# Kernel tuning notes

Hardware: AMD Instinct MI355X
Metric: run time of the kernel (lower is better)

The kernel has to match this reference:

```python
import jax, jax.numpy as jnp
import numpy as np
from jax import lax

B = 8192      # image batch
S = 32        # seq_length
I = 16        # ltc_input_size (sensory neurons)
U = 19        # ltc_hidden_size (units)
M = 2         # num_classes (motor neurons)
UNFOLDS = 6   # ncps LTCCell default ode_unfolds
EPS = 1e-8


def setup_inputs() -> dict:
    key = jax.random.key(0)
    ks = jax.random.split(key, 24)
    u = lambda k, sh, lo, hi: jax.random.uniform(k, sh, jnp.float32, lo, hi)
    x = jax.random.normal(ks[0], (B, 1, 28, 44), jnp.float32)
    conv1_w = jax.random.normal(ks[1], (6, 1, 5, 5), jnp.float32) * 0.2
    conv1_b = u(ks[2], (6,), -0.1, 0.1)
    conv2_w = jax.random.normal(ks[3], (16, 6, 5, 5), jnp.float32) * 0.08
    conv2_b = u(ks[4], (16,), -0.1, 0.1)
    # wiring adjacency (AutoNCP approximated by random sparse +/-1 polarity)
    sparsity_mask = (jax.random.uniform(ks[5], (U, U)) < 0.5).astype(jnp.float32)
    sensory_sparsity_mask = (jax.random.uniform(ks[6], (I, U)) < 0.5).astype(jnp.float32)
    erev = sparsity_mask * jnp.where(jax.random.uniform(ks[7], (U, U)) < 0.8, 1.0, -1.0)
    sensory_erev = sensory_sparsity_mask * jnp.where(jax.random.uniform(ks[8], (I, U)) < 0.8, 1.0, -1.0)
    # LTCCell parameter init ranges from ncps
    gleak = u(ks[9], (U,), 0.001, 1.0)
    vleak = u(ks[10], (U,), -0.2, 0.2)
    cm = u(ks[11], (U,), 0.4, 0.6)
    sigma = u(ks[12], (U, U), 3.0, 8.0)
    mu = u(ks[13], (U, U), 0.3, 0.8)
    w = u(ks[14], (U, U), 0.001, 1.0)
    sensory_sigma = u(ks[15], (I, U), 3.0, 8.0)
    sensory_mu = u(ks[16], (I, U), 0.3, 0.8)
    sensory_w = u(ks[17], (I, U), 0.001, 1.0)
    input_w = jnp.ones((I,), jnp.float32)
    input_b = jnp.zeros((I,), jnp.float32)
    output_w = jnp.ones((M,), jnp.float32)
    output_b = jnp.zeros((M,), jnp.float32)
    return dict(x=x, conv1_w=conv1_w, conv1_b=conv1_b, conv2_w=conv2_w, conv2_b=conv2_b,
                gleak=gleak, vleak=vleak, cm=cm, sigma=sigma, mu=mu, w=w, erev=erev,
                sensory_sigma=sensory_sigma, sensory_mu=sensory_mu, sensory_w=sensory_w,
                sensory_erev=sensory_erev, input_w=input_w, input_b=input_b,
                output_w=output_w, output_b=output_b,
                sparsity_mask=sparsity_mask, sensory_sparsity_mask=sensory_sparsity_mask)


def _maxpool2(h):
    return lax.reduce_window(h, -jnp.inf, lax.max, (1, 1, 2, 2), (1, 1, 2, 2), 'VALID')


def reference(x, conv1_w, conv1_b, conv2_w, conv2_b, gleak, vleak, cm, sigma, mu, w,
              erev, sensory_sigma, sensory_mu, sensory_w, sensory_erev, input_w, input_b,
              output_w, output_b, sparsity_mask, sensory_sparsity_mask):
    dn = ('NCHW', 'OIHW', 'NCHW')
    h = lax.conv_general_dilated(x, conv1_w, (1, 1), 'VALID', dimension_numbers=dn)
    h = _maxpool2(jax.nn.relu(h + conv1_b[None, :, None, None]))
    h = lax.conv_general_dilated(h, conv2_w, (1, 1), 'VALID', dimension_numbers=dn)
    h = _maxpool2(jax.nn.relu(h + conv2_b[None, :, None, None]))
    feat = h.reshape(h.shape[0], -1).reshape(-1, S, I)   # (B, 32, 16)
    seq = jnp.swapaxes(feat, 0, 1)                       # (S, B, I)
    cm_t = cm * UNFOLDS                                  # cm / (elapsed_time/unfolds), dt=1

    def step(v, inp):
        inp = inp * input_w + input_b                    # sensory affine mapping
        # sensory synapse activations (B, I, U), fixed over the ODE unfolds
        s_act = sensory_w * jax.nn.sigmoid(sensory_sigma * (inp[:, :, None] - sensory_mu))
        s_act = s_act * sensory_sparsity_mask
        w_num_s = jnp.sum(s_act * sensory_erev, axis=1)
        w_den_s = jnp.sum(s_act, axis=1)

        def unfold(vv, _):
            wa = w * jax.nn.sigmoid(sigma * (vv[:, :, None] - mu)) * sparsity_mask  # (B,U,U)
            num = cm_t * vv + gleak * vleak + jnp.sum(wa * erev, axis=1) + w_num_s
            den = cm_t + gleak + jnp.sum(wa, axis=1) + w_den_s
            return num / (den + EPS), None

        v, _ = lax.scan(unfold, v, None, length=UNFOLDS)
        return v, None

    v0 = jnp.zeros((feat.shape[0], U), x.dtype)
    vT, _ = lax.scan(step, v0, seq)
    # motor mapping: first M neurons, affine output map; equals out[:, -1, :]
    return vT[:, :M] * output_w + output_b
```

## Files before the change

### kernel.cpp

```cpp
#include <hip/hip_runtime.h>

#define BTOT 8192
#define SEQ 32
#define IPB 6
#define TPB 128
#define L2E 1.4426950408889634f
#define FSTRIDE 520
#define RSL 16


__global__ void prep_w2t(const float* __restrict__ w2, float* __restrict__ wt) {
    int idx = blockIdx.x * blockDim.x + threadIdx.x;
    if (idx < 2400) {
        int k = idx >> 4, c2 = idx & 15;
        wt[idx] = w2[c2 * 150 + k];
    }
}

__global__ void prep_params(
    const float* __restrict__ sigma, const float* __restrict__ mu,
    const float* __restrict__ ww, const float* __restrict__ erev,
    const float* __restrict__ ssigma, const float* __restrict__ smu,
    const float* __restrict__ sw, const float* __restrict__ serev,
    const float* __restrict__ inw, const float* __restrict__ inb,
    const float* __restrict__ mask, const float* __restrict__ smask,
    float* __restrict__ ws)
{
    __shared__ int ncol[19], mcol[19];
    float2* rAB = (float2*)(ws + 4096);
    float2* rZI = (float2*)(ws + 4864);
    float2* sAB = (float2*)(ws + 5632);
    float2* sZI = (float2*)(ws + 6240);
    int* cnt = (int*)(ws + 6848);
    const int j = threadIdx.x;
    if (j < 19) {
        for (int c = 0; c < 19; ++c) {
            rAB[c * 19 + j] = make_float2(0.f, 0.f);
            rZI[c * 19 + j] = make_float2(0.f, __int_as_float(0));
        }
        for (int c = 0; c < 16; ++c) {
            sAB[c * 19 + j] = make_float2(0.f, 0.f);
            sZI[c * 19 + j] = make_float2(0.f, __int_as_float(0));
        }
        int c = 0;
        for (int i = 0; i < 19; ++i) {
            int idx = i * 19 + j;
            if (mask[idx] != 0.f) {
                float s = sigma[idx];
                rAB[c * 19 + j] = make_float2(-L2E * s, L2E * s * mu[idx]);
                rZI[c * 19 + j] = make_float2(ww[idx] * erev[idx], __int_as_float(i));
                ++c;
            }
        }
        ncol[j] = c;
        c = 0;
        for (int i = 0; i < 16; ++i) {
            int idx = i * 19 + j;
            if (smask[idx] != 0.f) {
                float s = ssigma[idx];
                sAB[c * 19 + j] = make_float2(-L2E * s * inw[i],
                                              -L2E * s * (inb[i] - smu[idx]));
                sZI[c * 19 + j] = make_float2(sw[idx] * serev[idx], __int_as_float(i));
                ++c;
            }
        }
        mcol[j] = c;
    }
    __syncthreads();
    if (j == 0) {
        int MR = 0, MS = 0;
        for (int k = 0; k < 19; ++k) { MR = max(MR, ncol[k]); MS = max(MS, mcol[k]); }
        cnt[0] = MR;
        cnt[1] = MS;
    }
}

__global__ __launch_bounds__(128, 4) void conv_k(
    const float* __restrict__ xin,
    const float* __restrict__ w1, const float* __restrict__ b1,
    const float* __restrict__ b2, const float* __restrict__ wt,
    const float* __restrict__ sparam,
    const int* __restrict__ cnt,
    float2* __restrict__ wnwd)
{
    __shared__ __align__(16) float img[1232];
    __shared__ __align__(16) float c1p[1440];
    const int tid = threadIdx.x;
    const int bG = blockIdx.x;

    for (int idx = tid; idx < 1232; idx += 128) img[idx] = xin[bG * 1232 + idx];
    __syncthreads();
    for (int idx = tid; idx < 240; idx += 128) {
        int y = idx / 20, xx = idx - (idx / 20) * 20;
        const float* ib = img + (2 * y) * 44 + 2 * xx;
        float win[6][6];
        #pragma unroll
        for (int r = 0; r < 6; ++r) {
            float2 a = *(const float2*)(ib + r * 44);
            float2 b = *(const float2*)(ib + r * 44 + 2);
            float2 c = *(const float2*)(ib + r * 44 + 4);
            win[r][0] = a.x; win[r][1] = a.y; win[r][2] = b.x;
            win[r][3] = b.y; win[r][4] = c.x; win[r][5] = c.y;
        }
        for (int ch = 0; ch < 6; ++ch) {
            const float* wp = w1 + ch * 25;
            float a00 = 0.f, a01 = 0.f, a10 = 0.f, a11 = 0.f;
            #pragma unroll
            for (int ky = 0; ky < 5; ++ky)
                #pragma unroll
                for (int kx = 0; kx < 5; ++kx) {
                    float wv = wp[ky * 5 + kx];
                    a00 = fmaf(wv, win[ky][kx], a00);
                    a01 = fmaf(wv, win[ky][kx + 1], a01);
                    a10 = fmaf(wv, win[ky + 1][kx], a10);
                    a11 = fmaf(wv, win[ky + 1][kx + 1], a11);
                }
            float m = fmaxf(fmaxf(a00, a01), fmaxf(a10, a11)) + b1[ch];
            c1p[ch * 240 + idx] = fmaxf(m, 0.f);
        }
    }
    __syncthreads();
    {
        const int oy = tid >> 4, ox = tid & 15;
        float acc[16];
        #pragma unroll
        for (int c2 = 0; c2 < 16; ++c2) acc[c2] = 0.f;
        for (int ch = 0; ch < 6; ++ch) {
            const float* rowb = c1p + ch * 240 + oy * 20 + ox;
            const float* wch = wt + (ch * 25 << 4);
            #pragma unroll
            for (int ky = 0; ky < 5; ++ky) {
                #pragma unroll
                for (int kx = 0; kx < 5; ++kx) {
                    float xv = rowb[ky * 20 + kx];
                    const float4* wk = (const float4*)(wch + ((ky * 5 + kx) << 4));
                    float4 wa = wk[0], wb = wk[1], wc = wk[2], wd = wk[3];
                    acc[0]  = fmaf(wa.x, xv, acc[0]);  acc[1]  = fmaf(wa.y, xv, acc[1]);
                    acc[2]  = fmaf(wa.z, xv, acc[2]);  acc[3]  = fmaf(wa.w, xv, acc[3]);
                    acc[4]  = fmaf(wb.x, xv, acc[4]);  acc[5]  = fmaf(wb.y, xv, acc[5]);
                    acc[6]  = fmaf(wb.z, xv, acc[6]);  acc[7]  = fmaf(wb.w, xv, acc[7]);
                    acc[8]  = fmaf(wc.x, xv, acc[8]);  acc[9]  = fmaf(wc.y, xv, acc[9]);
                    acc[10] = fmaf(wc.z, xv, acc[10]); acc[11] = fmaf(wc.w, xv, acc[11]);
                    acc[12] = fmaf(wd.x, xv, acc[12]); acc[13] = fmaf(wd.y, xv, acc[13]);
                    acc[14] = fmaf(wd.z, xv, acc[14]); acc[15] = fmaf(wd.w, xv, acc[15]);
                }
            }
        }
        const bool wl = ((tid & 1) == 0) && ((tid & 16) == 0);
        const int obase = (oy >> 1) * 8 + (ox >> 1);
        #pragma unroll
        for (int c2 = 0; c2 < 16; ++c2) {
            float a = acc[c2];
            a = fmaxf(a, __shfl_xor(a, 1));
            a = fmaxf(a, __shfl_xor(a, 16));
            if (wl) img[obase + c2 * 32] = fmaxf(a + b2[c2], 0.f);
        }
    }
    __syncthreads();
    for (int idx = tid; idx < 1216; idx += 128) c1p[idx] = sparam[idx];
    __syncthreads();
    {
        const float2* sAB2 = (const float2*)c1p;
        const float2* sZI2 = (const float2*)(c1p + 608);
        const float* featI = img;
        const int MS = cnt[1];
        for (int p = tid; p < 608; p += 128) {
            int st = p / 19, j = p - (p / 19) * 19;
            float wn = 0.f, wd = 0.f;
            for (int c = 0; c < MS; ++c) {
                float2 ab = sAB2[c * 19 + j];
                float2 zi = sZI2[c * 19 + j];
                float f = featI[st * 16 + __float_as_int(zi.y)];
                float t = fmaf(ab.x, f, ab.y);
                float r = __builtin_amdgcn_rcpf(1.f + __builtin_amdgcn_exp2f(t));
                wn = fmaf(zi.x, r, wn);
                wd = fmaf(fabsf(zi.x), r, wd);
            }
            wnwd[(bG * SEQ + st) * 19 + j] = make_float2(wn, wd);
        }
    }
}

__global__ __launch_bounds__(64, 3) void ltc_k(
    const float2* __restrict__ wnwd,
    const float* __restrict__ rABg_, const float* __restrict__ rZIg_,
    const int* __restrict__ cnt,
    const float* __restrict__ gleak, const float* __restrict__ vleak,
    const float* __restrict__ cm,
    const float* __restrict__ outw, const float* __restrict__ outb,
    float* __restrict__ dout)
{
    const float2* rAB = (const float2*)rABg_;
    const float2* rZI = (const float2*)rZIg_;
    const int l = threadIdx.x;
    const int g = l / 19;
    const int j = l - g * 19;
    const int gbase = g * 19;
    const int b0 = blockIdx.x * 3;
    const bool act = (g < 3) && (b0 + g < BTOT);
    const int img = min(b0 + ((g < 3) ? g : 2), BTOT - 1);

    float UA[RSL], UB[RSL], UZ[RSL];
    int LI[RSL];
    #pragma unroll
    for (int c = 0; c < RSL; ++c) {
        float2 ab = rAB[c * 19 + j];
        float2 zi = rZI[c * 19 + j];
        UA[c] = ab.x; UB[c] = ab.y; UZ[c] = zi.x;
        LI[c] = gbase + __float_as_int(zi.y);
    }
    #pragma unroll
    for (int c = 0; c < RSL; ++c)
        asm volatile("" : "+v"(UA[c]), "+v"(UB[c]), "+v"(UZ[c]), "+v"(LI[c]));

    const int MR = cnt[0];
    const float gl = gleak[j];
    const float gv = gl * vleak[j];
    const float cmt = cm[j] * 6.f;

    float v = 0.f;
    const float2* wrow = wnwd + img * SEQ * 19 + j;
    float2 wcur = wrow[0];

    #pragma unroll 1
    for (int st = 0; st < SEQ; ++st) {
        float2 wnext = (st < SEQ - 1) ? wrow[(st + 1) * 19] : wcur;
        const float nb = gv + wcur.x;
        const float db = cmt + gl + wcur.y;
        #pragma unroll 1
        for (int u = 0; u < 6; ++u) {
            float n0 = fmaf(cmt, v, nb), n1 = 0.f;
            float d0 = db, d1 = 0.f;
            #pragma unroll
            for (int c = 0; c < RSL; ++c) {
                float vv = __shfl(v, LI[c]);
                float t = fmaf(UA[c], vv, UB[c]);
                float r = __builtin_amdgcn_rcpf(1.f + __builtin_amdgcn_exp2f(t));
                if (c & 1) { n1 = fmaf(UZ[c], r, n1); d1 = fmaf(fabsf(UZ[c]), r, d1); }
                else       { n0 = fmaf(UZ[c], r, n0); d0 = fmaf(fabsf(UZ[c]), r, d0); }
            }
            float num = n0 + n1;
            float den = d0 + d1;
            #pragma unroll 1
            for (int c = RSL; c < MR; ++c) {
                float2 ab = rAB[c * 19 + j];
                float2 zi = rZI[c * 19 + j];
                float vv = __shfl(v, gbase + __float_as_int(zi.y));
                float t = fmaf(ab.x, vv, ab.y);
                float r = __builtin_amdgcn_rcpf(1.f + __builtin_amdgcn_exp2f(t));
                num = fmaf(zi.x, r, num);
                den = fmaf(fabsf(zi.x), r, den);
            }
            v = num * __builtin_amdgcn_rcpf(den + 1e-8f);
        }
        wcur = wnext;
    }
    if (act && j < 2) dout[(b0 + g) * 2 + j] = fmaf(v, outw[j], outb[j]);
}

__global__ __launch_bounds__(TPB, 3) void ltc_fused(
    const float* __restrict__ xin,
    const float* __restrict__ w1, const float* __restrict__ b1,
    const float* __restrict__ b2,
    const float* __restrict__ gleak, const float* __restrict__ vleak, const float* __restrict__ cm,
    const float* __restrict__ sigma, const float* __restrict__ mu, const float* __restrict__ ww,
    const float* __restrict__ erev,
    const float* __restrict__ ssigma, const float* __restrict__ smu, const float* __restrict__ sw,
    const float* __restrict__ serev,
    const float* __restrict__ inw, const float* __restrict__ inb,
    const float* __restrict__ outw, const float* __restrict__ outb,
    const float* __restrict__ mask, const float* __restrict__ smask,
    const float* __restrict__ wt,
    float* __restrict__ dout)
{
    __shared__ __align__(16) float uni[2736];
    __shared__ __align__(16) float featL[IPB * FSTRIDE];
    __shared__ int ncol[19], mcol[19], cnts[2];

    float* img = uni;
    float* c1p = uni + 1232;
    float2* rAB = (float2*)uni;
    float2* rZI = (float2*)(uni + 760);
    float2* sAB = (float2*)(uni + 1520);
    float2* sZI = (float2*)(uni + 2128);

    const int tid = threadIdx.x;
    const int b0 = blockIdx.x * IPB;

    for (int k = 0; k < IPB; ++k) {
        const int bG = b0 + k;
        const bool valid = bG < BTOT;
        if (valid) {
            for (int idx = tid; idx < 1232; idx += TPB) img[idx] = xin[bG * 1232 + idx];
        }
        __syncthreads();
        if (valid) {
            for (int idx = tid; idx < 240; idx += TPB) {
                int y = idx / 20, xx = idx - (idx / 20) * 20;
                const float* ib = img + (2 * y) * 44 + 2 * xx;
                float win[6][6];
                #pragma unroll
                for (int r = 0; r < 6; ++r) {
                    float2 a = *(const float2*)(ib + r * 44);
                    float2 b = *(const float2*)(ib + r * 44 + 2);
                    float2 c = *(const float2*)(ib + r * 44 + 4);
                    win[r][0] = a.x; win[r][1] = a.y; win[r][2] = b.x;
                    win[r][3] = b.y; win[r][4] = c.x; win[r][5] = c.y;
                }
                for (int ch = 0; ch < 6; ++ch) {
                    const float* wp = w1 + ch * 25;
                    float a00 = 0.f, a01 = 0.f, a10 = 0.f, a11 = 0.f;
                    #pragma unroll
                    for (int ky = 0; ky < 5; ++ky)
                        #pragma unroll
                        for (int kx = 0; kx < 5; ++kx) {
                            float wv = wp[ky * 5 + kx];
                            a00 = fmaf(wv, win[ky][kx], a00);
                            a01 = fmaf(wv, win[ky][kx + 1], a01);
                            a10 = fmaf(wv, win[ky + 1][kx], a10);
                            a11 = fmaf(wv, win[ky + 1][kx + 1], a11);
                        }
                    float m = fmaxf(fmaxf(a00, a01), fmaxf(a10, a11)) + b1[ch];
                    c1p[ch * 240 + idx] = fmaxf(m, 0.f);
                }
            }
        }
        __syncthreads();
        if (valid) {
            const int oy = tid >> 4, ox = tid & 15;
            float acc[16];
            #pragma unroll
            for (int c2 = 0; c2 < 16; ++c2) acc[c2] = 0.f;
            for (int ch = 0; ch < 6; ++ch) {
                const float* rowb = c1p + ch * 240 + oy * 20 + ox;
                const float* wch = wt + (ch * 25 << 4);
                #pragma unroll
                for (int ky = 0; ky < 5; ++ky) {
                    #pragma unroll
                    for (int kx = 0; kx < 5; ++kx) {
                        float xv = rowb[ky * 20 + kx];
                        const float4* wk = (const float4*)(wch + ((ky * 5 + kx) << 4));
                        float4 wa = wk[0], wb = wk[1], wc = wk[2], wd = wk[3];
                        acc[0]  = fmaf(wa.x, xv, acc[0]);  acc[1]  = fmaf(wa.y, xv, acc[1]);
                        acc[2]  = fmaf(wa.z, xv, acc[2]);  acc[3]  = fmaf(wa.w, xv, acc[3]);
                        acc[4]  = fmaf(wb.x, xv, acc[4]);  acc[5]  = fmaf(wb.y, xv, acc[5]);
                        acc[6]  = fmaf(wb.z, xv, acc[6]);  acc[7]  = fmaf(wb.w, xv, acc[7]);
                        acc[8]  = fmaf(wc.x, xv, acc[8]);  acc[9]  = fmaf(wc.y, xv, acc[9]);
                        acc[10] = fmaf(wc.z, xv, acc[10]); acc[11] = fmaf(wc.w, xv, acc[11]);
                        acc[12] = fmaf(wd.x, xv, acc[12]); acc[13] = fmaf(wd.y, xv, acc[13]);
                        acc[14] = fmaf(wd.z, xv, acc[14]); acc[15] = fmaf(wd.w, xv, acc[15]);
                    }
                }
            }
            const bool wl = ((tid & 1) == 0) && ((tid & 16) == 0);
            const int obase = k * FSTRIDE + (oy >> 1) * 8 + (ox >> 1);
            #pragma unroll
            for (int c2 = 0; c2 < 16; ++c2) {
                float a = acc[c2];
                a = fmaxf(a, __shfl_xor(a, 1));
                a = fmaxf(a, __shfl_xor(a, 16));
                if (wl) featL[obase + c2 * 32] = fmaxf(a + b2[c2], 0.f);
            }
        }
        __syncthreads();
    }

    for (int idx = tid; idx < 2736; idx += TPB) uni[idx] = 0.f;
    __syncthreads();
    if (tid < 19) {
        const int jj = tid;
        int c = 0;
        for (int i = 0; i < 19; ++i) {
            int idx = i * 19 + jj;
            if (mask[idx] != 0.f) {
                float s = sigma[idx];
                rAB[c * 19 + jj] = make_float2(-L2E * s, L2E * s * mu[idx]);
                rZI[c * 19 + jj] = make_float2(ww[idx] * erev[idx], __int_as_float(i));
                ++c;
            }
        }
        ncol[jj] = c;
        c = 0;
        for (int i = 0; i < 16; ++i) {
            int idx = i * 19 + jj;
            if (smask[idx] != 0.f) {
                float s = ssigma[idx];
                sAB[c * 19 + jj] = make_float2(-L2E * s * inw[i],
                                               -L2E * s * (inb[i] - smu[idx]));
                sZI[c * 19 + jj] = make_float2(sw[idx] * serev[idx], __int_as_float(i));
                ++c;
            }
        }
        mcol[jj] = c;
    }
    __syncthreads();
    if (tid == 0) {
        int MRv = 0, MSv = 0;
        for (int j2 = 0; j2 < 19; ++j2) {
            MRv = max(MRv, ncol[j2]);
            MSv = max(MSv, mcol[j2]);
        }
        cnts[0] = MRv;
        cnts[1] = MSv;
    }
    __syncthreads();
    const int MR = __builtin_amdgcn_readfirstlane(cnts[0]);
    const int MS = __builtin_amdgcn_readfirstlane(cnts[1]);

    const int wv_ = tid >> 6, l = tid & 63;
    const int g = l / 19;
    const int j = l - g * 19;
    const int gbase = g * 19;
    const int kimg = wv_ * 3 + g;
    const bool act = (g < 3) && (b0 + kimg < BTOT);
    const int kc = (kimg < IPB) ? kimg : (IPB - 1);

    float UA[RSL], UB[RSL], UZ[RSL];
    int LI[RSL];
    #pragma unroll
    for (int c = 0; c < RSL; ++c) {
        float2 ab = rAB[c * 19 + j];
        float2 zi = rZI[c * 19 + j];
        UA[c] = ab.x; UB[c] = ab.y; UZ[c] = zi.x;
        LI[c] = gbase + __float_as_int(zi.y);
    }
    #pragma unroll
    for (int c = 0; c < RSL; ++c)
        asm volatile("" : "+v"(UA[c]), "+v"(UB[c]), "+v"(UZ[c]), "+v"(LI[c]));

    const float gl = gleak[j];
    const float gv = gl * vleak[j];
    const float cmt = cm[j] * 6.f;

    float v = 0.f;
    const float* frow = featL + kc * FSTRIDE;

    #pragma unroll 1
    for (int st = 0; st < SEQ; ++st) {
        const float* fb = frow + st * 16;
        float wns = 0.f, wds = 0.f;
        #pragma unroll 1
        for (int c = 0; c < MS; ++c) {
            float2 ab = sAB[c * 19 + j];
            float2 zi = sZI[c * 19 + j];
            float f = fb[__float_as_int(zi.y)];
            float t = fmaf(ab.x, f, ab.y);
            float r = __builtin_amdgcn_rcpf(1.f + __builtin_amdgcn_exp2f(t));
            wns = fmaf(zi.x, r, wns);
            wds = fmaf(fabsf(zi.x), r, wds);
        }
        const float nb = gv + wns;
        const float db = cmt + gl + wds;
        #pragma unroll 1
        for (int u = 0; u < 6; ++u) {
            float num = fmaf(cmt, v, nb);
            float den = db;
            #pragma unroll
            for (int c = 0; c < RSL; ++c) {
                float vv = __shfl(v, LI[c]);
                float t = fmaf(UA[c], vv, UB[c]);
                float r = __builtin_amdgcn_rcpf(1.f + __builtin_amdgcn_exp2f(t));
                num = fmaf(UZ[c], r, num);
                den = fmaf(fabsf(UZ[c]), r, den);
            }
            #pragma unroll 1
            for (int c = RSL; c < MR; ++c) {
                float2 ab = rAB[c * 19 + j];
                float2 zi = rZI[c * 19 + j];
                float vv = __shfl(v, gbase + __float_as_int(zi.y));
                float t = fmaf(ab.x, vv, ab.y);
                float r = __builtin_amdgcn_rcpf(1.f + __builtin_amdgcn_exp2f(t));
                num = fmaf(zi.x, r, num);
                den = fmaf(fabsf(zi.x), r, den);
            }
            v = num * __builtin_amdgcn_rcpf(den + 1e-8f);
        }
    }
    if (act && j < 2) dout[(b0 + kimg) * 2 + j] = fmaf(v, outw[j], outb[j]);
}

extern "C" void kernel_launch(void* const* d_in, const int* in_sizes, int n_in,
                              void* d_out, int out_size, void* d_ws, size_t ws_size,
                              hipStream_t stream) {
    const float* x      = (const float*)d_in[0];
    const float* w1     = (const float*)d_in[1];
    const float* b1     = (const float*)d_in[2];
    const float* w2     = (const float*)d_in[3];
    const float* b2     = (const float*)d_in[4];
    const float* gleak  = (const float*)d_in[5];
    const float* vleak  = (const float*)d_in[6];
    const float* cm     = (const float*)d_in[7];
    const float* sigma  = (const float*)d_in[8];
    const float* mu     = (const float*)d_in[9];
    const float* ww     = (const float*)d_in[10];
    const float* erev   = (const float*)d_in[11];
    const float* ssig   = (const float*)d_in[12];
    const float* smu    = (const float*)d_in[13];
    const float* sw     = (const float*)d_in[14];
    const float* serev  = (const float*)d_in[15];
    const float* inw    = (const float*)d_in[16];
    const float* inb    = (const float*)d_in[17];
    const float* outw   = (const float*)d_in[18];
    const float* outb   = (const float*)d_in[19];
    const float* mask   = (const float*)d_in[20];
    const float* smask  = (const float*)d_in[21];

    float* ws = (float*)d_ws;
    const size_t need = (size_t)(8192 + (size_t)BTOT * SEQ * 19 * 2) * 4;

    hipLaunchKernelGGL(prep_w2t, dim3(10), dim3(256), 0, stream, w2, ws);

    if (ws_size >= need) {
        hipLaunchKernelGGL(prep_params, dim3(1), dim3(64), 0, stream,
                           sigma, mu, ww, erev, ssig, smu, sw, serev, inw, inb,
                           mask, smask, ws);
        hipLaunchKernelGGL(conv_k, dim3(BTOT), dim3(128), 0, stream,
                           x, w1, b1, b2, (const float*)ws,
                           (const float*)(ws + 5632), (const int*)(ws + 6848),
                           (float2*)(ws + 8192));
        hipLaunchKernelGGL(ltc_k, dim3((BTOT + 2) / 3), dim3(64), 0, stream,
                           (const float2*)(ws + 8192),
                           (const float*)(ws + 4096), (const float*)(ws + 4864),
                           (const int*)(ws + 6848),
                           gleak, vleak, cm, outw, outb, (float*)d_out);
    } else {
        hipLaunchKernelGGL(ltc_fused, dim3((BTOT + IPB - 1) / IPB), dim3(TPB), 0, stream,
                           x, w1, b1, b2, gleak, vleak, cm, sigma, mu, ww, erev,
                           ssig, smu, sw, serev, inw, inb, outw, outb, mask, smask,
                           (const float*)ws, (float*)d_out);
    }
}
```

Before: 337.9 us.

## Restructure LTC recurrence to one image per wave with dense presynaptic split

The LTC kernel previously packed three images per 64-lane wave and walked a compacted sparse list of presynaptic synapses per neuron, reading neighbour voltages by lane shuffle. It now gives each wave a single image. The three 19-lane groups each cover 8 dense (zero-padded) presynaptic rows, read voltages from an LDS row with vector loads, and combine their partial sums by shuffle. Sigmoid pairs share one reciprocal via a cross-multiplied numerator. This trades more exp work on masked-out synapses and per-unfold LDS writes for shorter dependency chains, fewer shuffles and higher occupancy, at the cost of three times as many waves in total.

```diff
diff --git a/kernel.cpp b/kernel.cpp
--- a/kernel.cpp
+++ b/kernel.cpp
@@ -26,34 +26,32 @@
     const float* __restrict__ mask, const float* __restrict__ smask,
     float* __restrict__ ws)
 {
-    __shared__ int ncol[19], mcol[19];
-    float2* rAB = (float2*)(ws + 4096);
-    float2* rZI = (float2*)(ws + 4864);
+    __shared__ int mcol[19];
     float2* sAB = (float2*)(ws + 5632);
     float2* sZI = (float2*)(ws + 6240);
     int* cnt = (int*)(ws + 6848);
-    const int j = threadIdx.x;
-    if (j < 19) {
-        for (int c = 0; c < 19; ++c) {
-            rAB[c * 19 + j] = make_float2(0.f, 0.f);
-            rZI[c * 19 + j] = make_float2(0.f, __int_as_float(0));
-        }
+    float* Ap = ws + 7168;
+    float* Bp = ws + 7680;
+    float* Zp = ws + 8192;
+    const int t = threadIdx.x;
+    for (int idx = t; idx < 456; idx += 64) {
+        int i = idx / 19, j = idx - (idx / 19) * 19;
+        float a = 0.f, b = 0.f, z = 0.f;
+        if (i < 19 && mask[i * 19 + j] != 0.f) {
+            float s = sigma[i * 19 + j];
+            a = -L2E * s;
+            b = L2E * s * mu[i * 19 + j];
+            z = ww[i * 19 + j] * erev[i * 19 + j];
+        }
+        Ap[idx] = a; Bp[idx] = b; Zp[idx] = z;
+    }
+    if (t < 19) {
+        const int j = t;
         for (int c = 0; c < 16; ++c) {
             sAB[c * 19 + j] = make_float2(0.f, 0.f);
             sZI[c * 19 + j] = make_float2(0.f, __int_as_float(0));
         }
         int c = 0;
-        for (int i = 0; i < 19; ++i) {
-            int idx = i * 19 + j;
-            if (mask[idx] != 0.f) {
-                float s = sigma[idx];
-                rAB[c * 19 + j] = make_float2(-L2E * s, L2E * s * mu[idx]);
-                rZI[c * 19 + j] = make_float2(ww[idx] * erev[idx], __int_as_float(i));
-                ++c;
-            }
-        }
-        ncol[j] = c;
-        c = 0;
         for (int i = 0; i < 16; ++i) {
             int idx = i * 19 + j;
             if (smask[idx] != 0.f) {
@@ -67,10 +65,10 @@
         mcol[j] = c;
     }
     __syncthreads();
-    if (j == 0) {
-        int MR = 0, MS = 0;
-        for (int k = 0; k < 19; ++k) { MR = max(MR, ncol[k]); MS = max(MS, mcol[k]); }
-        cnt[0] = MR;
+    if (t == 0) {
+        int MS = 0;
+        for (int k = 0; k < 19; ++k) MS = max(MS, mcol[k]);
+        cnt[0] = 0;
         cnt[1] = MS;
     }
 }
@@ -181,44 +179,45 @@
     }
 }
 
-__global__ __launch_bounds__(64, 3) void ltc_k(
+__global__ __launch_bounds__(128, 6) void ltc_k2(
     const float2* __restrict__ wnwd,
-    const float* __restrict__ rABg_, const float* __restrict__ rZIg_,
-    const int* __restrict__ cnt,
+    const float* __restrict__ Ap, const float* __restrict__ Bp,
+    const float* __restrict__ Zp,
     const float* __restrict__ gleak, const float* __restrict__ vleak,
     const float* __restrict__ cm,
     const float* __restrict__ outw, const float* __restrict__ outb,
     float* __restrict__ dout)
 {
-    const float2* rAB = (const float2*)rABg_;
-    const float2* rZI = (const float2*)rZIg_;
-    const int l = threadIdx.x;
-    const int g = l / 19;
-    const int j = l - g * 19;
-    const int gbase = g * 19;
-    const int b0 = blockIdx.x * 3;
-    const bool act = (g < 3) && (b0 + g < BTOT);
-    const int img = min(b0 + ((g < 3) ? g : 2), BTOT - 1);
-
-    float UA[RSL], UB[RSL], UZ[RSL];
-    int LI[RSL];
+    __shared__ __align__(16) float vbuf[2][24];
+    const int tid = threadIdx.x;
+    const int wv = tid >> 6, l = tid & 63;
+    const int s3 = l / 19;
+    const int s = (s3 < 2) ? s3 : 2;
+    const int j = l - s3 * 19;
+    const int base = s * 8;
+    const int img = blockIdx.x * 2 + wv;
+
+    float A[8], Bb[8], Z[8];
     #pragma unroll
-    for (int c = 0; c < RSL; ++c) {
-        float2 ab = rAB[c * 19 + j];
-        float2 zi = rZI[c * 19 + j];
-        UA[c] = ab.x; UB[c] = ab.y; UZ[c] = zi.x;
-        LI[c] = gbase + __float_as_int(zi.y);
+    for (int c = 0; c < 8; ++c) {
+        A[c]  = Ap[(base + c) * 19 + j];
+        Bb[c] = Bp[(base + c) * 19 + j];
+        Z[c]  = Zp[(base + c) * 19 + j];
     }
     #pragma unroll
-    for (int c = 0; c < RSL; ++c)
-        asm volatile("" : "+v"(UA[c]), "+v"(UB[c]), "+v"(UZ[c]), "+v"(LI[c]));
-
-    const int MR = cnt[0];
+    for (int c = 0; c < 8; ++c)
+        asm volatile("" : "+v"(A[c]), "+v"(Bb[c]), "+v"(Z[c]));
+
     const float gl = gleak[j];
     const float gv = gl * vleak[j];
     const float cmt = cm[j] * 6.f;
 
     float v = 0.f;
+    float* vrow = &vbuf[wv][0];
+    if (l < 24) vrow[l] = 0.f;
+    __builtin_amdgcn_wave_barrier();
+    __asm__ volatile("" ::: "memory");
+
     const float2* wrow = wnwd + img * SEQ * 19 + j;
     float2 wcur = wrow[0];
 
@@ -229,33 +228,38 @@
         const float db = cmt + gl + wcur.y;
         #pragma unroll 1
         for (int u = 0; u < 6; ++u) {
-            float n0 = fmaf(cmt, v, nb), n1 = 0.f;
-            float d0 = db, d1 = 0.f;
+            float4 va = *(const float4*)(vrow + base);
+            float4 vbq = *(const float4*)(vrow + base + 4);
+            float vv[8] = {va.x, va.y, va.z, va.w, vbq.x, vbq.y, vbq.z, vbq.w};
+            float pn0 = 0.f, pd0 = 0.f, pn1 = 0.f, pd1 = 0.f;
             #pragma unroll
-            for (int c = 0; c < RSL; ++c) {
-                float vv = __shfl(v, LI[c]);
-                float t = fmaf(UA[c], vv, UB[c]);
-                float r = __builtin_amdgcn_rcpf(1.f + __builtin_amdgcn_exp2f(t));
-                if (c & 1) { n1 = fmaf(UZ[c], r, n1); d1 = fmaf(fabsf(UZ[c]), r, d1); }
-                else       { n0 = fmaf(UZ[c], r, n0); d0 = fmaf(fabsf(UZ[c]), r, d0); }
-            }
-            float num = n0 + n1;
-            float den = d0 + d1;
-            #pragma unroll 1
-            for (int c = RSL; c < MR; ++c) {
-                float2 ab = rAB[c * 19 + j];
-                float2 zi = rZI[c * 19 + j];
-                float vv = __shfl(v, gbase + __float_as_int(zi.y));
-                float t = fmaf(ab.x, vv, ab.y);
-                float r = __builtin_amdgcn_rcpf(1.f + __builtin_amdgcn_exp2f(t));
-                num = fmaf(zi.x, r, num);
-                den = fmaf(fabsf(zi.x), r, den);
-            }
+            for (int p = 0; p < 4; ++p) {
+                int c = p * 2;
+                float t0 = fmaf(A[c], vv[c], Bb[c]);
+                float t1 = fmaf(A[c + 1], vv[c + 1], Bb[c + 1]);
+                float q0 = 1.f + __builtin_amdgcn_exp2f(t0);
+                float q1 = 1.f + __builtin_amdgcn_exp2f(t1);
+                float rr = __builtin_amdgcn_rcpf(q0 * q1);
+                float cn = fmaf(Z[c], q1, Z[c + 1] * q0);
+                float cd = fmaf(fabsf(Z[c]), q1, fabsf(Z[c + 1]) * q0);
+                if (p & 1) { pn1 = fmaf(cn, rr, pn1); pd1 = fmaf(cd, rr, pd1); }
+                else       { pn0 = fmaf(cn, rr, pn0); pd0 = fmaf(cd, rr, pd0); }
+            }
+            float pn = pn0 + pn1, pd = pd0 + pd1;
+            float pnA = __shfl(pn, l + 19), pnB = __shfl(pn, l + 38);
+            float pdA = __shfl(pd, l + 19), pdB = __shfl(pd, l + 38);
+            float num = fmaf(cmt, v, nb) + (pn + pnA + pnB);
+            float den = db + (pd + pdA + pdB);
             v = num * __builtin_amdgcn_rcpf(den + 1e-8f);
+            __builtin_amdgcn_wave_barrier();
+            __asm__ volatile("" ::: "memory");
+            if (l < 19) vrow[l] = v;
+            __builtin_amdgcn_wave_barrier();
+            __asm__ volatile("" ::: "memory");
         }
         wcur = wnext;
     }
-    if (act && j < 2) dout[(b0 + g) * 2 + j] = fmaf(v, outw[j], outb[j]);
+    if (l < 2) dout[img * 2 + l] = fmaf(v, outw[l], outb[l]);
 }
 
 __global__ __launch_bounds__(TPB, 3) void ltc_fused(
@@ -506,7 +510,7 @@
     const float* smask  = (const float*)d_in[21];
 
     float* ws = (float*)d_ws;
-    const size_t need = (size_t)(8192 + (size_t)BTOT * SEQ * 19 * 2) * 4;
+    const size_t need = (size_t)(12288 + (size_t)BTOT * SEQ * 19 * 2) * 4;
 
     hipLaunchKernelGGL(prep_w2t, dim3(10), dim3(256), 0, stream, w2, ws);
 
@@ -517,11 +521,11 @@
         hipLaunchKernelGGL(conv_k, dim3(BTOT), dim3(128), 0, stream,
                            x, w1, b1, b2, (const float*)ws,
                            (const float*)(ws + 5632), (const int*)(ws + 6848),
-                           (float2*)(ws + 8192));
-        hipLaunchKernelGGL(ltc_k, dim3((BTOT + 2) / 3), dim3(64), 0, stream,
-                           (const float2*)(ws + 8192),
-                           (const float*)(ws + 4096), (const float*)(ws + 4864),
-                           (const int*)(ws + 6848),
+                           (float2*)(ws + 12288));
+        hipLaunchKernelGGL(ltc_k2, dim3(BTOT / 2), dim3(128), 0, stream,
+                           (const float2*)(ws + 12288),
+                           (const float*)(ws + 7168), (const float*)(ws + 7680),
+                           (const float*)(ws + 8192),
                            gleak, vleak, cm, outw, outb, (float*)d_out);
     } else {
         hipLaunchKernelGGL(ltc_fused, dim3((BTOT + IPB - 1) / IPB), dim3(TPB), 0, stream,
```

After: 346.1 us. 2.5% more time.
